# Optimization experiments

Hardware: AMD Instinct MI355X
Metric: run time of the kernel (lower is better)

Reference implementation:

```python
import jax, jax.numpy as jnp
import numpy as np

N_NODES = 100000


def gcn_conv(x, src, dst, W, b, n):
    # PyG GCNConv: add self-loops (weight 1), symmetric deg^-1/2 normalization,
    # linear transform, scatter-add to targets, then bias.
    loop = jnp.arange(n, dtype=src.dtype)
    s = jnp.concatenate([src, loop])
    d = jnp.concatenate([dst, loop])
    w = jnp.ones(s.shape[0], dtype=x.dtype)
    deg = jax.ops.segment_sum(w, d, num_segments=n)
    dis = jnp.where(deg > 0, jax.lax.rsqrt(deg), 0.0)
    norm = dis[s] * w * dis[d]                      # [E+N]
    h = x @ W                                       # [N, out]
    msg = h[s] * norm[:, None]                      # [E+N, out]
    out = jax.ops.segment_sum(msg, d, num_segments=n)
    return out + b


def setup_inputs() -> dict:
    key = jax.random.key(0)
    ks = jax.random.split(key, 8)
    num_node_types, emb_dim, hidden_dim, out_dim = 1000, 128, 128, 64
    n, e = N_NODES, 1600000
    x_node_types = jax.random.randint(ks[0], (n,), 0, num_node_types, dtype=jnp.int64 if jax.config.jax_enable_x64 else jnp.int32)
    edge_index = jax.random.randint(ks[1], (2, e), 0, n, dtype=x_node_types.dtype)
    emb = jax.random.normal(ks[2], (num_node_types, emb_dim), dtype=jnp.float32)
    W1 = jax.random.normal(ks[3], (emb_dim, hidden_dim), dtype=jnp.float32) / np.sqrt(emb_dim)
    b1 = jnp.zeros((hidden_dim,), dtype=jnp.float32)
    W2 = jax.random.normal(ks[4], (hidden_dim, out_dim), dtype=jnp.float32) / np.sqrt(hidden_dim)
    b2 = jnp.zeros((out_dim,), dtype=jnp.float32)
    return {"x_node_types": x_node_types, "edge_index": edge_index,
            "emb": emb, "W1": W1, "b1": b1, "W2": W2, "b2": b2}


def reference(x_node_types, edge_index, emb, W1, b1, W2, b2):
    n = N_NODES
    src, dst = edge_index[0], edge_index[1]
    x = emb[x_node_types]                           # embedding lookup [N, emb_dim]
    x = jax.nn.relu(gcn_conv(x, src, dst, W1, b1, n))
    # dropout p=0.5 is identity in eval mode (training=False)
    x = gcn_conv(x, src, dst, W2, b2, n)
    return x
```

## Files before the change

### kernel.cpp

```cpp
#include <hip/hip_runtime.h>
#include <hip/hip_bf16.h>


#define D1 128
#define D2 64
#define BSH 9
#define BW  512
#define BMAX 256
#define TILE 2048
#define SMASK 0x1FFFF

typedef __attribute__((ext_vector_type(8))) short short8v;
typedef __attribute__((ext_vector_type(4))) float f32x4;

__device__ __forceinline__ short bf16_hi(float x) {
    return (short)(__float_as_uint(x) >> 16);
}
__device__ __forceinline__ float hi_f(float x) {
    return __uint_as_float(__float_as_uint(x) & 0xFFFF0000u);
}
__device__ __forceinline__ short bf16_rne(float x) {
    unsigned u = __float_as_uint(x);
    return (short)((u + 0x7FFFu + ((u >> 16) & 1u)) >> 16);
}
__device__ __forceinline__ float bf16_f(unsigned short u) {
    return __uint_as_float((unsigned)u << 16);
}

__global__ __launch_bounds__(256) void bhist_k(const int* __restrict__ dst,
                                               int* __restrict__ bcnt, int e) {
    __shared__ int h[BMAX];
    if (threadIdx.x < BMAX) h[threadIdx.x] = 0;
    __syncthreads();
    int stride = gridDim.x * blockDim.x;
    for (int t = blockIdx.x * blockDim.x + threadIdx.x; t < e; t += stride)
        atomicAdd(&h[dst[t] >> BSH], 1);
    __syncthreads();
    if (threadIdx.x < BMAX && h[threadIdx.x])
        atomicAdd(&bcnt[threadIdx.x], h[threadIdx.x]);
}

__global__ void bscan_k(const int* __restrict__ bcnt, int* __restrict__ bbase,
                        int* __restrict__ bcur, int nb) {
    __shared__ int tmp[BMAX];
    int tid = threadIdx.x;
    int v = (tid < nb) ? bcnt[tid] : 0;
    tmp[tid] = v;
    __syncthreads();
    for (int s = 1; s < BMAX; s <<= 1) {
        int a = (tid >= s) ? tmp[tid - s] : 0;
        __syncthreads();
        tmp[tid] += a;
        __syncthreads();
    }
    if (tid < nb) { int ex = tmp[tid] - v; bbase[tid] = ex; bcur[tid] = ex; }
}

__global__ __launch_bounds__(256) void bpart_k(const int* __restrict__ src,
                                               const int* __restrict__ dst,
                                               int* __restrict__ bcur,
                                               unsigned* __restrict__ ebuf, int e) {
    __shared__ int hist[BMAX];
    __shared__ int chunk[BMAX];
    __shared__ int lcur[BMAX];
    int tid = threadIdx.x;
    int base = blockIdx.x * TILE;
    if (tid < BMAX) { hist[tid] = 0; lcur[tid] = 0; }
    __syncthreads();
    unsigned p8[8];
    int b8[8];
    #pragma unroll
    for (int i = 0; i < 8; ++i) {
        int t = base + i * 256 + tid;
        if (t < e) {
            int s = src[t], d = dst[t];
            b8[i] = d >> BSH;
            p8[i] = (unsigned)s | ((unsigned)(d & (BW - 1)) << 17);
            atomicAdd(&hist[b8[i]], 1);
        } else b8[i] = -1;
    }
    __syncthreads();
    if (tid < BMAX && hist[tid]) chunk[tid] = atomicAdd(&bcur[tid], hist[tid]);
    __syncthreads();
    #pragma unroll
    for (int i = 0; i < 8; ++i) {
        if (b8[i] >= 0) {
            int r = atomicAdd(&lcur[b8[i]], 1);
            ebuf[chunk[b8[i]] + r] = p8[i];
        }
    }
}

__global__ __launch_bounds__(512) void bcsr_k(const unsigned* __restrict__ ebuf,
                                              const int* __restrict__ bbase,
                                              const int* __restrict__ bcnt,
                                              const int* __restrict__ types,
                                              int* __restrict__ cnt,
                                              int* __restrict__ off,
                                              unsigned* __restrict__ csr, int n) {
    __shared__ int lcnt[BW];
    __shared__ int lsc[BW];
    __shared__ int lcur[BW];
    int b = blockIdx.x;
    int d0 = b << BSH;
    int tid = threadIdx.x;
    lcnt[tid] = 0; lcur[tid] = 0;
    __syncthreads();
    int ebase = bbase[b], ecnt = bcnt[b];
    for (int t = tid; t < ecnt; t += BW)
        atomicAdd(&lcnt[ebuf[ebase + t] >> 17], 1);
    __syncthreads();
    int v = lcnt[tid];
    lsc[tid] = v;
    __syncthreads();
    for (int s = 1; s < BW; s <<= 1) {
        int a = (tid >= s) ? lsc[tid - s] : 0;
        __syncthreads();
        lsc[tid] += a;
        __syncthreads();
    }
    int ex = lsc[tid] - v;
    int node = d0 + tid;
    if (node < n) { cnt[node] = v; off[node] = ebase + ex; }
    __syncthreads();
    lsc[tid] = ex;
    __syncthreads();
    for (int t = tid; t < ecnt; t += BW) {
        unsigned q = ebuf[ebase + t];
        int l = q >> 17;
        int s = q & SMASK;
        int r = atomicAdd(&lcur[l], 1);
        csr[ebase + lsc[l] + r] = (unsigned)s | ((unsigned)types[s] << 17);
    }
}

__global__ void dis_k(const int* __restrict__ cnt, float* __restrict__ dis, int n) {
    int stride = gridDim.x * blockDim.x;
    for (int t = blockIdx.x * blockDim.x + threadIdx.x; t < n; t += stride)
        dis[t] = rsqrtf((float)(cnt[t] + 1));
}

__global__ void w2prep_k(const float* __restrict__ W2,
                         short* __restrict__ w2h, short* __restrict__ w2l) {
    int t = blockIdx.x * blockDim.x + threadIdx.x;
    if (t >= D1 * D2) return;
    int k = t >> 6, c = t & 63;
    float v = W2[t];
    int ct = c >> 4, kb = k >> 5;
    int l = (((k >> 3) & 3) << 4) | (c & 15);
    int j = k & 7;
    int idx = (((ct << 2) | kb) * 64 + l) * 8 + j;
    w2h[idx] = bf16_hi(v);
    w2l[idx] = bf16_rne(v - hi_f(v));
}

__global__ __launch_bounds__(128) void gemm_emb_k(const float* __restrict__ emb,
                                                  const float* __restrict__ W1,
                                                  float* __restrict__ embW, int ntypes) {
    __shared__ float w[D1 * D1];
    for (int t = threadIdx.x; t < D1 * D1; t += 128) w[t] = W1[t];
    __syncthreads();
    int j = threadIdx.x;
    for (int r = blockIdx.x; r < ntypes; r += gridDim.x) {
        const float* er = emb + (size_t)r * D1;
        float acc = 0.f;
        #pragma unroll 8
        for (int k = 0; k < D1; ++k) acc = fmaf(er[k], w[k * D1 + j], acc);
        embW[(size_t)r * D1 + j] = acc;
    }
}

__global__ __launch_bounds__(256) void agg1_k(const int* __restrict__ types,
                                              const unsigned* __restrict__ csr,
                                              const int* __restrict__ off,
                                              const int* __restrict__ cnt,
                                              const float* __restrict__ dis,
                                              const float* __restrict__ embW,
                                              const float* __restrict__ b1,
                                              float* __restrict__ x1, int n) {
    int i = (blockIdx.x * blockDim.x + threadIdx.x) >> 6;
    if (i >= n) return;
    int lane = threadIdx.x & 63;
    int sub = lane >> 5;
    int fl = (lane & 31) << 2;
    float disi = dis[i];
    int ti = types[i];
    int base = off[i], c = cnt[i];
    int total = c + 1;
    float4 acc = make_float4(0.f, 0.f, 0.f, 0.f);
    for (int cb = 0; cb < total; cb += 64) {
        int idx = cb + lane;
        int t_l = 0;
        float c_l = 0.f;
        if (idx < c) {
            unsigned q = csr[base + idx];
            t_l = q >> 17;
            c_l = disi * dis[q & SMASK];
        } else if (idx == c) {
            t_l = ti;
            c_l = disi * disi;
        }
        int m = min(64, total - cb);
        for (int k0 = 0; k0 < m; k0 += 2) {
            int k = k0 + sub;
            int t = __shfl(t_l, k);
            float cf = __shfl(c_l, k);
            float4 v = *(const float4*)(embW + (size_t)t * D1 + fl);
            acc.x = fmaf(v.x, cf, acc.x);
            acc.y = fmaf(v.y, cf, acc.y);
            acc.z = fmaf(v.z, cf, acc.z);
            acc.w = fmaf(v.w, cf, acc.w);
        }
    }
    acc.x += __shfl_xor(acc.x, 32);
    acc.y += __shfl_xor(acc.y, 32);
    acc.z += __shfl_xor(acc.z, 32);
    acc.w += __shfl_xor(acc.w, 32);
    if (sub == 0) {
        float4 bv = ((const float4*)b1)[lane & 31];
        acc.x = fmaxf(acc.x + bv.x, 0.f);
        acc.y = fmaxf(acc.y + bv.y, 0.f);
        acc.z = fmaxf(acc.z + bv.z, 0.f);
        acc.w = fmaxf(acc.w + bv.w, 0.f);
        ((float4*)(x1 + (size_t)i * D1))[lane & 31] = acc;
    }
}

__global__ __launch_bounds__(256) void gemm2_k(const float* __restrict__ x1,
                                               const short* __restrict__ w2h,
                                               const short* __restrict__ w2l,
                                               unsigned short* __restrict__ h2b, int n) {
    int gw = (blockIdx.x * blockDim.x + threadIdx.x) >> 6;
    int lane = threadIdx.x & 63;
    int r0 = gw << 4;
    if (r0 >= n) return;
    int row = r0 + (lane & 15);
    int kq = lane >> 4;
    bool ok = row < n;
    const float* xr = x1 + (size_t)row * D1 + kq * 8;
    short8v ah[4], al[4];
    #pragma unroll
    for (int kb = 0; kb < 4; ++kb) {
        float4 v0, v1;
        if (ok) {
            v0 = *(const float4*)(xr + kb * 32);
            v1 = *(const float4*)(xr + kb * 32 + 4);
        } else {
            v0 = make_float4(0.f, 0.f, 0.f, 0.f);
            v1 = v0;
        }
        float xv[8] = {v0.x, v0.y, v0.z, v0.w, v1.x, v1.y, v1.z, v1.w};
        #pragma unroll
        for (int j = 0; j < 8; ++j) {
            ah[kb][j] = bf16_hi(xv[j]);
            al[kb][j] = bf16_rne(xv[j] - hi_f(xv[j]));
        }
    }
    const short8v* w2hv = (const short8v*)w2h;
    const short8v* w2lv = (const short8v*)w2l;
    #pragma unroll
    for (int ct = 0; ct < 4; ++ct) {
        f32x4 acc = {0.f, 0.f, 0.f, 0.f};
        #pragma unroll
        for (int kb = 0; kb < 4; ++kb) {
            short8v bh = w2hv[(ct * 4 + kb) * 64 + lane];
            short8v bl = w2lv[(ct * 4 + kb) * 64 + lane];
            acc = __builtin_amdgcn_mfma_f32_16x16x32_bf16(ah[kb], bh, acc, 0, 0, 0);
            acc = __builtin_amdgcn_mfma_f32_16x16x32_bf16(al[kb], bh, acc, 0, 0, 0);
            acc = __builtin_amdgcn_mfma_f32_16x16x32_bf16(ah[kb], bl, acc, 0, 0, 0);
        }
        #pragma unroll
        for (int v = 0; v < 4; ++v) {
            int orow = r0 + (lane >> 4) * 4 + v;
            if (orow < n)
                h2b[(size_t)orow * D2 + ct * 16 + (lane & 15)] =
                    (unsigned short)bf16_rne(acc[v]);
        }
    }
}

__global__ __launch_bounds__(256) void agg2_k(const unsigned* __restrict__ csr,
                                              const int* __restrict__ off,
                                              const int* __restrict__ cnt,
                                              const float* __restrict__ dis,
                                              const unsigned short* __restrict__ h2b,
                                              const float* __restrict__ b2,
                                              float* __restrict__ out, int n) {
    int i = (blockIdx.x * blockDim.x + threadIdx.x) >> 6;
    if (i >= n) return;
    int lane = threadIdx.x & 63;
    int sub = lane >> 4;
    int fl = (lane & 15) << 2;
    float disi = dis[i];
    int base = off[i], c = cnt[i];
    int total = c + 1;
    float4 acc = make_float4(0.f, 0.f, 0.f, 0.f);
    for (int cb = 0; cb < total; cb += 64) {
        int idx = cb + lane;
        int s_l = i;
        float c_l = 0.f;
        if (idx < c) {
            unsigned q = csr[base + idx];
            s_l = q & SMASK;
            c_l = disi * dis[s_l];
        } else if (idx == c) {
            c_l = disi * disi;
        }
        int m = min(64, total - cb);
        for (int k0 = 0; k0 < m; k0 += 4) {
            int k = k0 + sub;
            int s = __shfl(s_l, k);
            float cf = __shfl(c_l, k);
            ushort4 hv = *(const ushort4*)(h2b + (size_t)s * D2 + fl);
            acc.x = fmaf(bf16_f(hv.x), cf, acc.x);
            acc.y = fmaf(bf16_f(hv.y), cf, acc.y);
            acc.z = fmaf(bf16_f(hv.z), cf, acc.z);
            acc.w = fmaf(bf16_f(hv.w), cf, acc.w);
        }
    }
    acc.x += __shfl_xor(acc.x, 16);
    acc.y += __shfl_xor(acc.y, 16);
    acc.z += __shfl_xor(acc.z, 16);
    acc.w += __shfl_xor(acc.w, 16);
    acc.x += __shfl_xor(acc.x, 32);
    acc.y += __shfl_xor(acc.y, 32);
    acc.z += __shfl_xor(acc.z, 32);
    acc.w += __shfl_xor(acc.w, 32);
    if (sub == 0) {
        float4 bv = ((const float4*)b2)[lane & 15];
        acc.x += bv.x;
        acc.y += bv.y;
        acc.z += bv.z;
        acc.w += bv.w;
        ((float4*)(out + (size_t)i * D2))[lane & 15] = acc;
    }
}

extern "C" void kernel_launch(void* const* d_in, const int* in_sizes, int n_in,
                              void* d_out, int out_size, void* d_ws, size_t ws_size,
                              hipStream_t stream) {
    const int* types = (const int*)d_in[0];
    const int* edges = (const int*)d_in[1];
    const float* emb = (const float*)d_in[2];
    const float* W1  = (const float*)d_in[3];
    const float* b1  = (const float*)d_in[4];
    const float* W2  = (const float*)d_in[5];
    const float* b2  = (const float*)d_in[6];
    float* out = (float*)d_out;

    const int n = in_sizes[0];
    const int e = in_sizes[1] / 2;
    const int ntypes = in_sizes[2] / D1;
    const int* src = edges;
    const int* dst = edges + e;
    const int nb = (n + BW - 1) >> BSH;

    char* p = (char*)d_ws;
    auto alloc = [&](size_t bytes) {
        char* r = p;
        p += (bytes + 255) & ~(size_t)255;
        return r;
    };
    int*      bcnt  = (int*)      alloc(BMAX * 4);
    int*      bbase = (int*)      alloc(BMAX * 4);
    int*      bcur  = (int*)      alloc(BMAX * 4);
    int*      cnt   = (int*)      alloc((size_t)n * 4);
    int*      off   = (int*)      alloc((size_t)n * 4);
    float*    dis   = (float*)    alloc((size_t)n * 4);
    short*    w2h   = (short*)    alloc((size_t)D1 * D2 * 2);
    short*    w2l   = (short*)    alloc((size_t)D1 * D2 * 2);
    unsigned* ebuf  = (unsigned*) alloc((size_t)e * 4);
    unsigned* csr   = (unsigned*) alloc((size_t)e * 4);
    float*    embW  = (float*)    alloc((size_t)ntypes * D1 * 4);
    float*    x1    = (float*)    alloc((size_t)n * D1 * 4);
    unsigned short* h2b = (unsigned short*)alloc((size_t)n * D2 * 2);
    (void)ws_size;

    hipMemsetAsync(bcnt, 0, BMAX * 4, stream);

    bhist_k<<<512, 256, 0, stream>>>(dst, bcnt, e);
    bscan_k<<<1, BMAX, 0, stream>>>(bcnt, bbase, bcur, nb);
    bpart_k<<<(e + TILE - 1) / TILE, 256, 0, stream>>>(src, dst, bcur, ebuf, e);
    bcsr_k<<<nb, BW, 0, stream>>>(ebuf, bbase, bcnt, types, cnt, off, csr, n);
    dis_k<<<(n + 255) / 256, 256, 0, stream>>>(cnt, dis, n);
    w2prep_k<<<(D1 * D2 + 255) / 256, 256, 0, stream>>>(W2, w2h, w2l);

    gemm_emb_k<<<256, 128, 0, stream>>>(emb, W1, embW, ntypes);
    int nwb = (n + 3) / 4;
    agg1_k<<<nwb, 256, 0, stream>>>(types, csr, off, cnt, dis, embW, b1, x1, n);

    int ngw = (n + 15) / 16;
    gemm2_k<<<(ngw + 3) / 4, 256, 0, stream>>>(x1, w2h, w2l, h2b, n);
    agg2_k<<<nwb, 256, 0, stream>>>(csr, off, cnt, dis, h2b, b2, out, n);
}
```

Measured before the change: 293.7 us.

## Precompute per-edge norm coefficients into CSR and unroll gather loops

Splits CSR construction into a count kernel (which also computes deg^-1/2, replacing the separate dis kernel) and a fill kernel that stores each edge as an int2 of packed source/type plus its precomputed normalization coefficient. Both aggregation kernels then read the coefficient directly instead of doing a random gather of dis[src] per edge. The inner gather loops are unrolled 4x with two accumulators to put more loads in flight. In exchange, CSR storage doubles to 8 bytes per edge, so both aggregations read more edge bytes, and the build now makes a second pass over ebuf.

```diff
diff --git a/kernel.cpp b/kernel.cpp
--- a/kernel.cpp
+++ b/kernel.cpp
@@ -91,20 +91,18 @@
     }
 }
 
-__global__ __launch_bounds__(512) void bcsr_k(const unsigned* __restrict__ ebuf,
-                                              const int* __restrict__ bbase,
-                                              const int* __restrict__ bcnt,
-                                              const int* __restrict__ types,
-                                              int* __restrict__ cnt,
-                                              int* __restrict__ off,
-                                              unsigned* __restrict__ csr, int n) {
+__global__ __launch_bounds__(512) void bcsr_count_k(const unsigned* __restrict__ ebuf,
+                                                    const int* __restrict__ bbase,
+                                                    const int* __restrict__ bcnt,
+                                                    int* __restrict__ cnt,
+                                                    int* __restrict__ off,
+                                                    float* __restrict__ dis, int n) {
     __shared__ int lcnt[BW];
     __shared__ int lsc[BW];
-    __shared__ int lcur[BW];
     int b = blockIdx.x;
     int d0 = b << BSH;
     int tid = threadIdx.x;
-    lcnt[tid] = 0; lcur[tid] = 0;
+    lcnt[tid] = 0;
     __syncthreads();
     int ebase = bbase[b], ecnt = bcnt[b];
     for (int t = tid; t < ecnt; t += BW)
@@ -119,25 +117,40 @@
         lsc[tid] += a;
         __syncthreads();
     }
-    int ex = lsc[tid] - v;
     int node = d0 + tid;
-    if (node < n) { cnt[node] = v; off[node] = ebase + ex; }
-    __syncthreads();
-    lsc[tid] = ex;
-    __syncthreads();
+    if (node < n) {
+        cnt[node] = v;
+        off[node] = ebase + lsc[tid] - v;
+        dis[node] = rsqrtf((float)(v + 1));
+    }
+}
+
+__global__ __launch_bounds__(512) void bcsr_fill_k(const unsigned* __restrict__ ebuf,
+                                                   const int* __restrict__ bbase,
+                                                   const int* __restrict__ bcnt,
+                                                   const int* __restrict__ off,
+                                                   const float* __restrict__ dis,
+                                                   const int* __restrict__ types,
+                                                   int2* __restrict__ csr_p, int n) {
+    __shared__ int loff[BW];
+    __shared__ float ldis[BW];
+    __shared__ int lcur[BW];
+    int b = blockIdx.x;
+    int d0 = b << BSH;
+    int tid = threadIdx.x;
+    int node = d0 + tid;
+    lcur[tid] = 0;
+    if (node < n) { loff[tid] = off[node]; ldis[tid] = dis[node]; }
+    __syncthreads();
+    int ebase = bbase[b], ecnt = bcnt[b];
     for (int t = tid; t < ecnt; t += BW) {
         unsigned q = ebuf[ebase + t];
         int l = q >> 17;
         int s = q & SMASK;
         int r = atomicAdd(&lcur[l], 1);
-        csr[ebase + lsc[l] + r] = (unsigned)s | ((unsigned)types[s] << 17);
-    }
-}
-
-__global__ void dis_k(const int* __restrict__ cnt, float* __restrict__ dis, int n) {
-    int stride = gridDim.x * blockDim.x;
-    for (int t = blockIdx.x * blockDim.x + threadIdx.x; t < n; t += stride)
-        dis[t] = rsqrtf((float)(cnt[t] + 1));
+        float coef = ldis[l] * dis[s];
+        csr_p[loff[l] + r] = make_int2(s | (types[s] << 17), __float_as_int(coef));
+    }
 }
 
 __global__ void w2prep_k(const float* __restrict__ W2,
@@ -171,7 +184,7 @@
 }
 
 __global__ __launch_bounds__(256) void agg1_k(const int* __restrict__ types,
-                                              const unsigned* __restrict__ csr,
+                                              const int2* __restrict__ csr_p,
                                               const int* __restrict__ off,
                                               const int* __restrict__ cnt,
                                               const float* __restrict__ dis,
@@ -184,34 +197,56 @@
     int sub = lane >> 5;
     int fl = (lane & 31) << 2;
     float disi = dis[i];
-    int ti = types[i];
     int base = off[i], c = cnt[i];
     int total = c + 1;
-    float4 acc = make_float4(0.f, 0.f, 0.f, 0.f);
-    for (int cb = 0; cb < total; cb += 64) {
-        int idx = cb + lane;
+    float4 a0 = make_float4(0.f, 0.f, 0.f, 0.f);
+    float4 a1 = make_float4(0.f, 0.f, 0.f, 0.f);
+    for (int cbk = 0; cbk < total; cbk += 64) {
+        int idx = cbk + lane;
         int t_l = 0;
         float c_l = 0.f;
         if (idx < c) {
-            unsigned q = csr[base + idx];
-            t_l = q >> 17;
-            c_l = disi * dis[q & SMASK];
+            int2 q = csr_p[base + idx];
+            t_l = q.x >> 17;
+            c_l = __int_as_float(q.y);
         } else if (idx == c) {
-            t_l = ti;
+            t_l = types[i];
             c_l = disi * disi;
         }
-        int m = min(64, total - cb);
-        for (int k0 = 0; k0 < m; k0 += 2) {
+        int m = min(64, total - cbk);
+        int k0 = 0;
+        for (; k0 + 8 <= m; k0 += 8) {
+            int   tA = __shfl(t_l, k0 + sub);
+            float cA = __shfl(c_l, k0 + sub);
+            int   tB = __shfl(t_l, k0 + 2 + sub);
+            float cB = __shfl(c_l, k0 + 2 + sub);
+            int   tC = __shfl(t_l, k0 + 4 + sub);
+            float cC = __shfl(c_l, k0 + 4 + sub);
+            int   tD = __shfl(t_l, k0 + 6 + sub);
+            float cD = __shfl(c_l, k0 + 6 + sub);
+            float4 vA = *(const float4*)(embW + (size_t)tA * D1 + fl);
+            float4 vB = *(const float4*)(embW + (size_t)tB * D1 + fl);
+            float4 vC = *(const float4*)(embW + (size_t)tC * D1 + fl);
+            float4 vD = *(const float4*)(embW + (size_t)tD * D1 + fl);
+            a0.x = fmaf(vA.x, cA, a0.x); a0.y = fmaf(vA.y, cA, a0.y);
+            a0.z = fmaf(vA.z, cA, a0.z); a0.w = fmaf(vA.w, cA, a0.w);
+            a1.x = fmaf(vB.x, cB, a1.x); a1.y = fmaf(vB.y, cB, a1.y);
+            a1.z = fmaf(vB.z, cB, a1.z); a1.w = fmaf(vB.w, cB, a1.w);
+            a0.x = fmaf(vC.x, cC, a0.x); a0.y = fmaf(vC.y, cC, a0.y);
+            a0.z = fmaf(vC.z, cC, a0.z); a0.w = fmaf(vC.w, cC, a0.w);
+            a1.x = fmaf(vD.x, cD, a1.x); a1.y = fmaf(vD.y, cD, a1.y);
+            a1.z = fmaf(vD.z, cD, a1.z); a1.w = fmaf(vD.w, cD, a1.w);
+        }
+        for (; k0 < m; k0 += 2) {
             int k = k0 + sub;
-            int t = __shfl(t_l, k);
+            int   t = __shfl(t_l, k);
             float cf = __shfl(c_l, k);
             float4 v = *(const float4*)(embW + (size_t)t * D1 + fl);
-            acc.x = fmaf(v.x, cf, acc.x);
-            acc.y = fmaf(v.y, cf, acc.y);
-            acc.z = fmaf(v.z, cf, acc.z);
-            acc.w = fmaf(v.w, cf, acc.w);
-        }
-    }
+            a0.x = fmaf(v.x, cf, a0.x); a0.y = fmaf(v.y, cf, a0.y);
+            a0.z = fmaf(v.z, cf, a0.z); a0.w = fmaf(v.w, cf, a0.w);
+        }
+    }
+    float4 acc = make_float4(a0.x + a1.x, a0.y + a1.y, a0.z + a1.z, a0.w + a1.w);
     acc.x += __shfl_xor(acc.x, 32);
     acc.y += __shfl_xor(acc.y, 32);
     acc.z += __shfl_xor(acc.z, 32);
@@ -279,7 +314,7 @@
     }
 }
 
-__global__ __launch_bounds__(256) void agg2_k(const unsigned* __restrict__ csr,
+__global__ __launch_bounds__(256) void agg2_k(const int2* __restrict__ csr_p,
                                               const int* __restrict__ off,
                                               const int* __restrict__ cnt,
                                               const float* __restrict__ dis,
@@ -294,30 +329,53 @@
     float disi = dis[i];
     int base = off[i], c = cnt[i];
     int total = c + 1;
-    float4 acc = make_float4(0.f, 0.f, 0.f, 0.f);
-    for (int cb = 0; cb < total; cb += 64) {
-        int idx = cb + lane;
+    float4 a0 = make_float4(0.f, 0.f, 0.f, 0.f);
+    float4 a1 = make_float4(0.f, 0.f, 0.f, 0.f);
+    for (int cbk = 0; cbk < total; cbk += 64) {
+        int idx = cbk + lane;
         int s_l = i;
         float c_l = 0.f;
         if (idx < c) {
-            unsigned q = csr[base + idx];
-            s_l = q & SMASK;
-            c_l = disi * dis[s_l];
+            int2 q = csr_p[base + idx];
+            s_l = q.x & SMASK;
+            c_l = __int_as_float(q.y);
         } else if (idx == c) {
             c_l = disi * disi;
         }
-        int m = min(64, total - cb);
-        for (int k0 = 0; k0 < m; k0 += 4) {
+        int m = min(64, total - cbk);
+        int k0 = 0;
+        for (; k0 + 16 <= m; k0 += 16) {
+            int   sA = __shfl(s_l, k0 + sub);
+            float cA = __shfl(c_l, k0 + sub);
+            int   sB = __shfl(s_l, k0 + 4 + sub);
+            float cB = __shfl(c_l, k0 + 4 + sub);
+            int   sC = __shfl(s_l, k0 + 8 + sub);
+            float cC = __shfl(c_l, k0 + 8 + sub);
+            int   sD = __shfl(s_l, k0 + 12 + sub);
+            float cD = __shfl(c_l, k0 + 12 + sub);
+            ushort4 hA = *(const ushort4*)(h2b + (size_t)sA * D2 + fl);
+            ushort4 hB = *(const ushort4*)(h2b + (size_t)sB * D2 + fl);
+            ushort4 hC = *(const ushort4*)(h2b + (size_t)sC * D2 + fl);
+            ushort4 hD = *(const ushort4*)(h2b + (size_t)sD * D2 + fl);
+            a0.x = fmaf(bf16_f(hA.x), cA, a0.x); a0.y = fmaf(bf16_f(hA.y), cA, a0.y);
+            a0.z = fmaf(bf16_f(hA.z), cA, a0.z); a0.w = fmaf(bf16_f(hA.w), cA, a0.w);
+            a1.x = fmaf(bf16_f(hB.x), cB, a1.x); a1.y = fmaf(bf16_f(hB.y), cB, a1.y);
+            a1.z = fmaf(bf16_f(hB.z), cB, a1.z); a1.w = fmaf(bf16_f(hB.w), cB, a1.w);
+            a0.x = fmaf(bf16_f(hC.x), cC, a0.x); a0.y = fmaf(bf16_f(hC.y), cC, a0.y);
+            a0.z = fmaf(bf16_f(hC.z), cC, a0.z); a0.w = fmaf(bf16_f(hC.w), cC, a0.w);
+            a1.x = fmaf(bf16_f(hD.x), cD, a1.x); a1.y = fmaf(bf16_f(hD.y), cD, a1.y);
+            a1.z = fmaf(bf16_f(hD.z), cD, a1.z); a1.w = fmaf(bf16_f(hD.w), cD, a1.w);
+        }
+        for (; k0 < m; k0 += 4) {
             int k = k0 + sub;
-            int s = __shfl(s_l, k);
+            int   s = __shfl(s_l, k);
             float cf = __shfl(c_l, k);
             ushort4 hv = *(const ushort4*)(h2b + (size_t)s * D2 + fl);
-            acc.x = fmaf(bf16_f(hv.x), cf, acc.x);
-            acc.y = fmaf(bf16_f(hv.y), cf, acc.y);
-            acc.z = fmaf(bf16_f(hv.z), cf, acc.z);
-            acc.w = fmaf(bf16_f(hv.w), cf, acc.w);
-        }
-    }
+            a0.x = fmaf(bf16_f(hv.x), cf, a0.x); a0.y = fmaf(bf16_f(hv.y), cf, a0.y);
+            a0.z = fmaf(bf16_f(hv.z), cf, a0.z); a0.w = fmaf(bf16_f(hv.w), cf, a0.w);
+        }
+    }
+    float4 acc = make_float4(a0.x + a1.x, a0.y + a1.y, a0.z + a1.z, a0.w + a1.w);
     acc.x += __shfl_xor(acc.x, 16);
     acc.y += __shfl_xor(acc.y, 16);
     acc.z += __shfl_xor(acc.z, 16);
@@ -370,7 +428,7 @@
     short*    w2h   = (short*)    alloc((size_t)D1 * D2 * 2);
     short*    w2l   = (short*)    alloc((size_t)D1 * D2 * 2);
     unsigned* ebuf  = (unsigned*) alloc((size_t)e * 4);
-    unsigned* csr   = (unsigned*) alloc((size_t)e * 4);
+    int2*     csr_p = (int2*)     alloc((size_t)e * 8);
     float*    embW  = (float*)    alloc((size_t)ntypes * D1 * 4);
     float*    x1    = (float*)    alloc((size_t)n * D1 * 4);
     unsigned short* h2b = (unsigned short*)alloc((size_t)n * D2 * 2);
@@ -381,15 +439,15 @@
     bhist_k<<<512, 256, 0, stream>>>(dst, bcnt, e);
     bscan_k<<<1, BMAX, 0, stream>>>(bcnt, bbase, bcur, nb);
     bpart_k<<<(e + TILE - 1) / TILE, 256, 0, stream>>>(src, dst, bcur, ebuf, e);
-    bcsr_k<<<nb, BW, 0, stream>>>(ebuf, bbase, bcnt, types, cnt, off, csr, n);
-    dis_k<<<(n + 255) / 256, 256, 0, stream>>>(cnt, dis, n);
+    bcsr_count_k<<<nb, BW, 0, stream>>>(ebuf, bbase, bcnt, cnt, off, dis, n);
+    bcsr_fill_k<<<nb, BW, 0, stream>>>(ebuf, bbase, bcnt, off, dis, types, csr_p, n);
     w2prep_k<<<(D1 * D2 + 255) / 256, 256, 0, stream>>>(W2, w2h, w2l);
 
     gemm_emb_k<<<256, 128, 0, stream>>>(emb, W1, embW, ntypes);
     int nwb = (n + 3) / 4;
-    agg1_k<<<nwb, 256, 0, stream>>>(types, csr, off, cnt, dis, embW, b1, x1, n);
+    agg1_k<<<nwb, 256, 0, stream>>>(types, csr_p, off, cnt, dis, embW, b1, x1, n);
 
     int ngw = (n + 15) / 16;
     gemm2_k<<<(ngw + 3) / 4, 256, 0, stream>>>(x1, w2h, w2l, h2b, n);
-    agg2_k<<<nwb, 256, 0, stream>>>(csr, off, cnt, dis, h2b, b2, out, n);
-}
+    agg2_k<<<nwb, 256, 0, stream>>>(csr_p, off, cnt, dis, h2b, b2, out, n);
+}
```

Measured after the change: 283.2 us. 1.04x faster.
